# Optimization experiments

Hardware: AMD Instinct MI355X
Metric: run time of the kernel (lower is better)

## Reference

```python
import jax, jax.numpy as jnp
import numpy as np

HEADS = 8
HC = 64  # num_head_channels
DIM = 256
HIDDEN = HEADS * HC
EPS = 1e-5


def setup_inputs() -> dict:
    key = jax.random.key(0)
    ks = jax.random.split(key, 6)
    x = jax.random.normal(ks[0], (16, DIM, 64, 64), dtype=jnp.float32)
    Wq = jax.random.normal(ks[1], (HIDDEN, DIM), dtype=jnp.float32) * 0.02
    Wk = jax.random.normal(ks[2], (HIDDEN, DIM), dtype=jnp.float32) * 0.02
    Wv = jax.random.normal(ks[3], (HIDDEN, DIM), dtype=jnp.float32) * 0.02
    Wo = jax.random.normal(ks[4], (DIM, HIDDEN), dtype=jnp.float32) * 0.02
    bo = jnp.zeros((DIM,), dtype=jnp.float32)
    gamma = jnp.ones((DIM,), dtype=jnp.float32)
    beta = jnp.zeros((DIM,), dtype=jnp.float32)
    return {"x": x, "Wq": Wq, "Wk": Wk, "Wv": Wv, "Wo": Wo, "bo": bo,
            "gamma": gamma, "beta": beta}


def reference(x, Wq, Wk, Wv, Wo, bo, gamma, beta):
    b, c, h, w = x.shape
    n = h * w
    scale = HC ** (-0.5)
    xf = x.reshape(b, c, n)  # [b, c, n]
    # 1x1 convs == channel matmuls
    q = jnp.einsum('oc,bcn->bon', Wq, xf).reshape(b * HEADS, HC, n)
    k = jnp.einsum('oc,bcn->bon', Wk, xf).reshape(b * HEADS, HC, n)
    v = jnp.einsum('oc,bcn->bon', Wv, xf).reshape(b * HEADS, HC, n)
    q = jax.nn.softmax(q, axis=1) * scale      # softmax over head channels
    k = jax.nn.softmax(k, axis=2)              # softmax over spatial
    # context = k @ v^T : [bh, hc, hc]
    context = jnp.einsum('bdn,ben->bde', k, v)
    # output = context^T @ q : [bh, hc, n]
    out = jnp.einsum('bde,bdn->ben', context, q)
    out = out.reshape(b, HIDDEN, n)
    # to_out conv1x1 + bias
    y = jnp.einsum('oc,bcn->bon', Wo, out) + bo[None, :, None]
    # GroupNorm(num_groups=1): normalize over (c, n) per sample
    mean = jnp.mean(y, axis=(1, 2), keepdims=True)
    var = jnp.var(y, axis=(1, 2), keepdims=True)
    y = (y - mean) * jax.lax.rsqrt(var + EPS)
    y = y * gamma[None, :, None] + beta[None, :, None]
    return y.reshape(b, c, h, w) + x
```

## Files before the change

### kernel.cpp

```cpp
#include <hip/hip_runtime.h>
#include <hip/hip_bf16.h>

#define DEV __device__ __forceinline__

constexpr int B_ = 16, CDIM = 256, NDIM = 4096, HID = 512, HEADS = 8, HC = 64;
constexpr float EPSV = 1e-5f;

using bf16x8 = __attribute__((ext_vector_type(8))) __bf16;
using f32x4  = __attribute__((ext_vector_type(4))) float;
using s16x8  = __attribute__((ext_vector_type(8))) short;
using s16x4  = __attribute__((ext_vector_type(4))) short;

DEV short f2bf(float f) {
  __hip_bfloat16 h = __float2bfloat16(f);
  return *reinterpret_cast<short*>(&h);
}
DEV float bf2f(short s) {
  union { unsigned u; float f; } c;
  c.u = ((unsigned)(unsigned short)s) << 16;
  return c.f;
}
DEV f32x4 MFMA(bf16x8 a, bf16x8 b, f32x4 c) {
  return __builtin_amdgcn_mfma_f32_16x16x32_bf16(a, b, c, 0, 0, 0);
}

__global__ void wconv_kernel(const float* __restrict__ Wq, const float* __restrict__ Wk,
                             const float* __restrict__ Wv, const float* __restrict__ Wo,
                             short* __restrict__ Wall, short* __restrict__ Wo_b) {
  const int i = blockIdx.x * 256 + threadIdx.x;
  const int nw = HID * CDIM;
  if (i < nw) Wall[i] = f2bf(Wq[i]);
  else if (i < 2 * nw) Wall[i] = f2bf(Wk[i - nw]);
  else if (i < 3 * nw) Wall[i] = f2bf(Wv[i - 2 * nw]);
  if (i < CDIM * HID) Wo_b[i] = f2bf(Wo[i]);
}

__global__ __launch_bounds__(256) void xconv_kernel(const float* __restrict__ x, short* __restrict__ xt) {
  __shared__ float t[32][33];
  const int bi = blockIdx.z, n0 = blockIdx.x * 32, c0 = blockIdx.y * 32;
  const int tx = threadIdx.x, ty = threadIdx.y;
  const float* xb = x + (size_t)bi * CDIM * NDIM;
#pragma unroll
  for (int i = 0; i < 32; i += 8)
    t[ty + i][tx] = xb[(size_t)(c0 + ty + i) * NDIM + n0 + tx];
  __syncthreads();
  short* xtb = xt + (size_t)bi * NDIM * CDIM;
#pragma unroll
  for (int i = 0; i < 32; i += 8)
    xtb[(size_t)(n0 + ty + i) * CDIM + c0 + tx] = f2bf(t[tx][ty + i]);
}

DEV bf16x8 xs_read(const char* xs, int row, int colShorts) {
  int byte = (row << 9) + (colShorts << 1);
  byte ^= (row & 7) << 4;
  return *(const bf16x8*)(xs + byte);
}
DEV bf16x8 t128_read(const char* t, int row, int colShorts) {
  int byte = (row << 7) + (colShorts << 1);
  byte ^= (row & 7) << 4;
  return *(const bf16x8*)(t + byte);
}

__global__ __launch_bounds__(256) void kvslice_kernel(const short* __restrict__ Wall,
                                                      const short* __restrict__ xt,
                                                      float* __restrict__ ctxp,
                                                      float* __restrict__ statp,
                                                      int nper) {
  const int phys = blockIdx.x, sl = blockIdx.y, nsl = gridDim.y;
  const int h = phys >> 4, bi = phys & 15;
  const int bh = bi * 8 + h;
  const int tid = threadIdx.x, lane = tid & 63, wid = tid >> 6;
  const int ro = lane & 15, g = lane >> 4, ko = g * 8;
  const short* Wk = Wall + (size_t)(HID + h * HC) * CDIM;
  const short* Wv = Wall + (size_t)(2 * HID + h * HC) * CDIM;
  const char* xbase = (const char*)(xt + ((size_t)bi * NDIM + (size_t)sl * nper) * CDIM);
  __shared__ __align__(16) char xs[64 * 512];
  __shared__ short pl[64][68];
  __shared__ short vl[64][68];
  bf16x8 ak[8], av[8];
#pragma unroll
  for (int ks = 0; ks < 8; ++ks) {
    ak[ks] = *(const bf16x8*)&Wk[(size_t)(wid * 16 + ro) * CDIM + ks * 32 + ko];
    av[ks] = *(const bf16x8*)&Wv[(size_t)(wid * 16 + ro) * CDIM + ks * 32 + ko];
  }
  float ssum = 0.f;
  f32x4 cacc[4] = {};
  const int myrow = wid * 16 + ro;
  const int drow = wid * 16 + g * 4;
  s16x8 r[8];
#pragma unroll
  for (int it = 0; it < 8; ++it) r[it] = *(const s16x8*)(xbase + it * 4096 + tid * 16);
  for (int nc = 0; nc < nper; nc += 64) {
    if (nc > 0) {
#pragma unroll
      for (int ks = 0; ks < 2; ++ks) {
        bf16x8 pa = *(const bf16x8*)&pl[wid * 16 + ro][ks * 32 + ko];
#pragma unroll
        for (int et = 0; et < 4; ++et) {
          bf16x8 vb = *(const bf16x8*)&vl[et * 16 + ro][ks * 32 + ko];
          cacc[et] = MFMA(pa, vb, cacc[et]);
        }
      }
    }
#pragma unroll
    for (int it = 0; it < 8; ++it) {
      const int fb = it * 4096 + tid * 16;
      *(s16x8*)(xs + (fb ^ (((fb >> 9) & 7) << 4))) = r[it];
    }
    __syncthreads();
    if (nc + 64 < nper) {
      const char* srcn = xbase + (size_t)(nc + 64) * 512;
#pragma unroll
      for (int it = 0; it < 8; ++it) r[it] = *(const s16x8*)(srcn + it * 4096 + tid * 16);
    }
    f32x4 kacc[4] = {};
    f32x4 vacc[4] = {};
#pragma unroll
    for (int ks = 0; ks < 8; ++ks)
#pragma unroll
      for (int nt = 0; nt < 4; ++nt) {
        bf16x8 bfr = xs_read(xs, nt * 16 + ro, ks * 32 + ko);
        kacc[nt] = MFMA(bfr, ak[ks], kacc[nt]);
        vacc[nt] = MFMA(bfr, av[ks], vacc[nt]);
      }
#pragma unroll
    for (int nt = 0; nt < 4; ++nt) {
      s16x4 pv, vv;
#pragma unroll
      for (int j = 0; j < 4; ++j) {
        const float p = __expf(kacc[nt][j]);
        ssum += p;
        pv[j] = f2bf(p);
        vv[j] = f2bf(vacc[nt][j]);
      }
      *(s16x4*)&pl[myrow][nt * 16 + g * 4] = pv;
      *(s16x4*)&vl[myrow][nt * 16 + g * 4] = vv;
    }
    __syncthreads();
  }
#pragma unroll
  for (int ks = 0; ks < 2; ++ks) {
    bf16x8 pa = *(const bf16x8*)&pl[wid * 16 + ro][ks * 32 + ko];
#pragma unroll
    for (int et = 0; et < 4; ++et) {
      bf16x8 vb = *(const bf16x8*)&vl[et * 16 + ro][ks * 32 + ko];
      cacc[et] = MFMA(pa, vb, cacc[et]);
    }
  }
  ssum += __shfl_xor(ssum, 16);
  ssum += __shfl_xor(ssum, 32);
  float* cp = ctxp + ((size_t)bh * nsl + sl) * HC * HC;
#pragma unroll
  for (int et = 0; et < 4; ++et)
#pragma unroll
    for (int j = 0; j < 4; ++j)
      cp[(drow + j) * HC + et * 16 + ro] = cacc[et][j];
  if (g == 0) {
    float* sp = statp + ((size_t)bh * nsl + sl) * HC;
    sp[myrow] = ssum;
  }
}

__global__ __launch_bounds__(256) void qsm_kernel(const short* __restrict__ Wall,
                                                  const short* __restrict__ xt,
                                                  short* __restrict__ qtc,
                                                  int NC, int nbase) {
  const int bi = blockIdx.y, n0 = blockIdx.x * 64;
  const int tid = threadIdx.x, lane = tid & 63, wid = tid >> 6;
  const int ro = lane & 15, g = lane >> 4, ko = g * 8;
  __shared__ __align__(16) char xs[64 * 512];
  __shared__ short qtile[64][68];
  __shared__ float ps[4][4][16];
  const char* xbase = (const char*)(xt + ((size_t)bi * NDIM + nbase + n0) * CDIM);
#pragma unroll
  for (int it = 0; it < 8; ++it) {
    const int fb = it * 4096 + tid * 16;
    *(s16x8*)(xs + (fb ^ (((fb >> 9) & 7) << 4))) = *(const s16x8*)(xbase + fb);
  }
  __syncthreads();
  const short* wbase = Wall + (size_t)(wid * 16 + ro) * CDIM + ko;
  bf16x8 aq[8], aqn[8];
#pragma unroll
  for (int ks = 0; ks < 8; ++ks) aq[ks] = *(const bf16x8*)(wbase + ks * 32);
#pragma unroll 1
  for (int h = 0; h < HEADS; ++h) {
    if (h < 7) {
      const short* wn = wbase + (size_t)(h + 1) * HC * CDIM;
#pragma unroll
      for (int ks = 0; ks < 8; ++ks) aqn[ks] = *(const bf16x8*)(wn + ks * 32);
    }
    f32x4 kacc[4] = {};
#pragma unroll
    for (int ks = 0; ks < 8; ++ks)
#pragma unroll
      for (int nt = 0; nt < 4; ++nt)
        kacc[nt] = MFMA(aq[ks], xs_read(xs, nt * 16 + ro, ks * 32 + ko), kacc[nt]);
    float tsum[4];
#pragma unroll
    for (int nt = 0; nt < 4; ++nt) {
#pragma unroll
      for (int j = 0; j < 4; ++j) kacc[nt][j] = __expf(kacc[nt][j]);
      tsum[nt] = kacc[nt][0] + kacc[nt][1] + kacc[nt][2] + kacc[nt][3];
    }
#pragma unroll
    for (int nt = 0; nt < 4; ++nt) {
      tsum[nt] += __shfl_xor(tsum[nt], 16);
      tsum[nt] += __shfl_xor(tsum[nt], 32);
    }
    if (g == 0) {
#pragma unroll
      for (int nt = 0; nt < 4; ++nt) ps[wid][nt][ro] = tsum[nt];
    }
#pragma unroll
    for (int nt = 0; nt < 4; ++nt) {
      s16x4 v;
#pragma unroll
      for (int j = 0; j < 4; ++j) v[j] = f2bf(kacc[nt][j]);
      *(s16x4*)&qtile[nt * 16 + ro][wid * 16 + g * 4] = v;
    }
    __syncthreads();
    {
      const int row = tid >> 2, cb = (tid & 3) * 16;
      const int ntr = row >> 4, ror = row & 15;
      const float t = ps[0][ntr][ror] + ps[1][ntr][ror] + ps[2][ntr][ror] + ps[3][ntr][ror];
      const float inv = 0.125f / t;
      short* dst = qtc + ((size_t)bi * NC + n0 + row) * HID + h * HC + cb;
      s16x8 o0, o1;
#pragma unroll
      for (int jj = 0; jj < 8; ++jj) o0[jj] = f2bf(bf2f(qtile[row][cb + jj]) * inv);
#pragma unroll
      for (int jj = 0; jj < 8; ++jj) o1[jj] = f2bf(bf2f(qtile[row][cb + 8 + jj]) * inv);
      *(s16x8*)dst = o0;
      *(s16x8*)(dst + 8) = o1;
    }
    __syncthreads();
#pragma unroll
    for (int ks = 0; ks < 8; ++ks) aq[ks] = aqn[ks];
  }
}

__global__ __launch_bounds__(256) void cmred_kernel(const float* __restrict__ ctxp,
                                                    const float* __restrict__ statp,
                                                    const short* __restrict__ Wo_b,
                                                    short* __restrict__ Meff, int nsl) {
  const int bh = blockIdx.x, bi = bh >> 3, h = bh & 7;
  const int tid = threadIdx.x, lane = tid & 63, wid = tid >> 6;
  const int ro = lane & 15, ko = (lane >> 4) * 8;
  __shared__ short cl[64][68];
  {
    const int d = tid >> 2, eb = (tid & 3) * 16;
    const float* sp = statp + (size_t)bh * nsl * HC;
    float stot = 0.f;
    for (int i = 0; i < nsl; ++i) stot += sp[i * HC + d];
    const float inv = 1.f / stot;
    const float* cp = ctxp + (size_t)bh * nsl * HC * HC + d * HC + eb;
#pragma unroll
    for (int e4 = 0; e4 < 16; e4 += 4) {
      float u0 = 0.f, u1 = 0.f, u2 = 0.f, u3 = 0.f;
      for (int i = 0; i < nsl; ++i) {
        const float4 c = *(const float4*)&cp[i * HC * HC + e4];
        u0 += c.x; u1 += c.y; u2 += c.z; u3 += c.w;
      }
      cl[d][eb + e4 + 0] = f2bf(u0 * inv);
      cl[d][eb + e4 + 1] = f2bf(u1 * inv);
      cl[d][eb + e4 + 2] = f2bf(u2 * inv);
      cl[d][eb + e4 + 3] = f2bf(u3 * inv);
    }
  }
  __syncthreads();
  const short* Arow = Wo_b + h * HC;
  f32x4 acc[4][4] = {};
#pragma unroll
  for (int ks = 0; ks < 64; ks += 32) {
    bf16x8 af[4], bv[4];
#pragma unroll
    for (int mi = 0; mi < 4; ++mi)
      af[mi] = *(const bf16x8*)&Arow[(size_t)(wid * 64 + mi * 16 + ro) * HID + ks + ko];
#pragma unroll
    for (int ni = 0; ni < 4; ++ni)
      bv[ni] = *(const bf16x8*)&cl[ni * 16 + ro][ks + ko];
#pragma unroll
    for (int mi = 0; mi < 4; ++mi)
#pragma unroll
      for (int ni = 0; ni < 4; ++ni) acc[mi][ni] = MFMA(af[mi], bv[ni], acc[mi][ni]);
  }
  short* Mb = Meff + (size_t)bi * CDIM * HID + h * HC;
  const int r0 = wid * 64 + ((lane >> 4) << 2), c0 = lane & 15;
#pragma unroll
  for (int mi = 0; mi < 4; ++mi)
#pragma unroll
    for (int ni = 0; ni < 4; ++ni)
#pragma unroll
      for (int j = 0; j < 4; ++j)
        Mb[(size_t)(r0 + mi * 16 + j) * HID + ni * 16 + c0] = f2bf(acc[mi][ni][j]);
}

template <bool BF16OUT>
__global__ __launch_bounds__(256) void ymm_kernel(const short* __restrict__ Meff,
                                                  const short* __restrict__ qtc,
                                                  const float* __restrict__ bo,
                                                  void* __restrict__ yout,
                                                  float2* __restrict__ partials,
                                                  int NC, int nbase, int pbase, int swz) {
  constexpr int K = HID;
  __shared__ __align__(16) char Al[128 * 128];
  __shared__ __align__(16) char Bl[128 * 128];
  __shared__ float a1[4], a2[4];
  int bi, mt, nt;
  if (swz) {
    const int lin = blockIdx.x + 32 * blockIdx.y + 64 * blockIdx.z;
    bi = ((lin & 7) << 1) | (lin >> 9);
    const int rest = (lin >> 3) & 63;
    mt = rest >> 5;
    nt = rest & 31;
  } else {
    bi = blockIdx.z; mt = blockIdx.y; nt = blockIdx.x;
  }
  const int tid = threadIdx.x, lane = tid & 63, wid = tid >> 6;
  const int wr = (wid >> 1) * 64, wc = (wid & 1) * 64;
  const char* Ab = (const char*)(Meff + (size_t)bi * CDIM * HID + (size_t)mt * 128 * K);
  const char* Bb = (const char*)(qtc + ((size_t)bi * NC + (size_t)nt * 128) * K);
  f32x4 acc[4][4] = {};
  const int ro = lane & 15, ko = (lane >> 4) * 8;
  for (int kt = 0; kt < K; kt += 64) {
    const char* As = Ab + kt * 2;
    const char* Bs = Bb + kt * 2;
#pragma unroll
    for (int it = 0; it < 4; ++it) {
      const int fb = it * 4096 + tid * 16;
      const int row = fb >> 7, inner = fb & 127;
      const int swb = fb ^ ((row & 7) << 4);
      *(s16x8*)(Al + swb) = *(const s16x8*)(As + (size_t)row * 1024 + inner);
      *(s16x8*)(Bl + swb) = *(const s16x8*)(Bs + (size_t)row * 1024 + inner);
    }
    __syncthreads();
#pragma unroll
    for (int ks = 0; ks < 64; ks += 32) {
      bf16x8 af[4], bfr[4];
#pragma unroll
      for (int i = 0; i < 4; ++i) {
        af[i]  = t128_read(Al, wr + i * 16 + ro, ks + ko);
        bfr[i] = t128_read(Bl, wc + i * 16 + ro, ks + ko);
      }
#pragma unroll
      for (int mi = 0; mi < 4; ++mi)
#pragma unroll
        for (int ni = 0; ni < 4; ++ni)
          acc[mi][ni] = MFMA(af[mi], bfr[ni], acc[mi][ni]);
    }
    __syncthreads();
  }
  const int r0 = mt * 128 + wr + ((lane >> 4) << 2);
  const int c0 = nbase + nt * 128 + wc + ro;
  float s1 = 0.f, s2 = 0.f;
#pragma unroll
  for (int mi = 0; mi < 4; ++mi)
#pragma unroll
    for (int j = 0; j < 4; ++j) {
      const int row = r0 + mi * 16 + j;
      const float b = bo[row];
#pragma unroll
      for (int ni = 0; ni < 4; ++ni) {
        const float v = acc[mi][ni][j] + b;
        if constexpr (BF16OUT)
          ((short*)yout)[(size_t)bi * CDIM * NDIM + (size_t)row * NDIM + c0 + ni * 16] = f2bf(v);
        else
          ((float*)yout)[(size_t)bi * CDIM * NDIM + (size_t)row * NDIM + c0 + ni * 16] = v;
        s1 += v;
        s2 += v * v;
      }
    }
#pragma unroll
  for (int o = 1; o < 64; o <<= 1) { s1 += __shfl_xor(s1, o); s2 += __shfl_xor(s2, o); }
  if (lane == 0) { a1[wid] = s1; a2[wid] = s2; }
  __syncthreads();
  if (tid == 0)
    partials[bi * 64 + pbase + mt * gridDim.x + nt] =
        make_float2(a1[0] + a1[1] + a1[2] + a1[3], a2[0] + a2[1] + a2[2] + a2[3]);
}

__global__ void redstats_kernel(const float2* __restrict__ partials, float* __restrict__ stats) {
  const int bi = blockIdx.x, l = threadIdx.x;
  float2 p = partials[bi * 64 + l];
  float s1 = p.x, s2 = p.y;
#pragma unroll
  for (int o = 32; o; o >>= 1) { s1 += __shfl_xor(s1, o); s2 += __shfl_xor(s2, o); }
  if (l == 0) { stats[bi * 2] = s1; stats[bi * 2 + 1] = s2; }
}

template <bool YBF>
__global__ __launch_bounds__(256) void final_kernel(const void* __restrict__ ysrc, float* __restrict__ dst,
                                                    const float* __restrict__ x,
                                                    const float* __restrict__ gamma, const float* __restrict__ beta,
                                                    const float* __restrict__ stats) {
  const int bi = blockIdx.y;
  constexpr float invN = 1.f / ((float)CDIM * NDIM);
  const float mean = stats[bi * 2] * invN;
  const float var = stats[bi * 2 + 1] * invN - mean * mean;
  const float rstd = rsqrtf(var + EPSV);
  float4* d4 = (float4*)(dst + (size_t)bi * CDIM * NDIM);
  const float4* x4 = (const float4*)(x + (size_t)bi * CDIM * NDIM);
  for (int i = blockIdx.x * 256 + threadIdx.x; i < CDIM * NDIM / 4; i += 128 * 256) {
    const int c = i >> 10;
    const float g = gamma[c] * rstd;
    const float b = beta[c] - mean * g;
    float4 v;
    if constexpr (YBF) {
      s16x4 yv = *(const s16x4*)((const short*)ysrc + (size_t)bi * CDIM * NDIM + (size_t)i * 4);
      v.x = bf2f(yv[0]); v.y = bf2f(yv[1]); v.z = bf2f(yv[2]); v.w = bf2f(yv[3]);
    } else {
      v = ((const float4*)((const float*)ysrc + (size_t)bi * CDIM * NDIM))[i];
    }
    const float4 xv = x4[i];
    v.x = v.x * g + b + xv.x;
    v.y = v.y * g + b + xv.y;
    v.z = v.z * g + b + xv.z;
    v.w = v.w * g + b + xv.w;
    d4[i] = v;
  }
}

extern "C" void kernel_launch(void* const* d_in, const int* in_sizes, int n_in,
                              void* d_out, int out_size, void* d_ws, size_t ws_size,
                              hipStream_t stream) {
  const float* x     = (const float*)d_in[0];
  const float* Wq    = (const float*)d_in[1];
  const float* Wk    = (const float*)d_in[2];
  const float* Wv    = (const float*)d_in[3];
  const float* Wo    = (const float*)d_in[4];
  const float* bo    = (const float*)d_in[5];
  const float* gamma = (const float*)d_in[6];
  const float* beta  = (const float*)d_in[7];
  float* out = (float*)d_out;

  char* w = (char*)d_ws;
  size_t off = 0;
  auto alloc = [&](size_t n) {
    char* p = w + off;
    off = (off + n + 255) & ~(size_t)255;
    return p;
  };
  constexpr int NSL = 8;
  short* xt    = (short*)alloc((size_t)B_ * NDIM * CDIM * 2);
  short* Wall  = (short*)alloc((size_t)3 * HID * CDIM * 2);
  short* Wo_b  = (short*)alloc((size_t)CDIM * HID * 2);
  short* Meff  = (short*)alloc((size_t)B_ * CDIM * HID * 2);
  float2* partials = (float2*)alloc((size_t)B_ * 64 * sizeof(float2));
  float* stats = (float*)alloc(32 * 4);
  float* ctxp  = (float*)alloc((size_t)128 * NSL * HC * HC * 4);
  float* statp = (float*)alloc((size_t)128 * NSL * HC * 4);
  const size_t base = off;

  int NC = 4096;
  while (NC > 64 && base + (size_t)B_ * NC * HID * 2 > ws_size) NC >>= 1;
  short* qtc = (short*)alloc((size_t)B_ * NC * HID * 2);
  const size_t ybf_bytes = (size_t)B_ * CDIM * NDIM * 2;
  const bool use_ybf = (off + ybf_bytes) <= ws_size;
  short* ybf = use_ybf ? (short*)alloc(ybf_bytes) : nullptr;

  wconv_kernel<<<1536, 256, 0, stream>>>(Wq, Wk, Wv, Wo, Wall, Wo_b);
  xconv_kernel<<<dim3(128, 8, B_), dim3(32, 8), 0, stream>>>(x, xt);
  kvslice_kernel<<<dim3(128, NSL), 256, 0, stream>>>(Wall, xt, ctxp, statp, NDIM / NSL);
  cmred_kernel<<<128, 256, 0, stream>>>(ctxp, statp, Wo_b, Meff, NSL);
  const int nchunks = NDIM / NC;
  for (int c = 0; c < nchunks; ++c) {
    const int swz = (NC == 4096) ? 1 : 0;
    qsm_kernel<<<dim3(NC / 64, B_), 256, 0, stream>>>(Wall, xt, qtc, NC, c * NC);
    if (use_ybf)
      ymm_kernel<true><<<dim3(NC / 128, 2, B_), 256, 0, stream>>>(Meff, qtc, bo, ybf, partials,
                                                                  NC, c * NC, c * 2 * (NC / 128), swz);
    else
      ymm_kernel<false><<<dim3(NC / 128, 2, B_), 256, 0, stream>>>(Meff, qtc, bo, out, partials,
                                                                   NC, c * NC, c * 2 * (NC / 128), swz);
  }
  redstats_kernel<<<B_, 64, 0, stream>>>(partials, stats);
  if (use_ybf)
    final_kernel<true><<<dim3(128, B_), 256, 0, stream>>>(ybf, out, x, gamma, beta, stats);
  else
    final_kernel<false><<<dim3(128, B_), 256, 0, stream>>>(out, out, x, gamma, beta, stats);
}
```

Measured before the change: 190.3 us.

## Fuse q-softmax projection into output matmul and add MFMA priority hints

Replaces the separate q-softmax kernel and the Meff×q output matmul with one fused kernel. Each block computes q for a 64-column tile over two head groups, keeps the normalized q in LDS, and multiplies by Meff directly, so the large qtc intermediate is never written to or read from global memory. It also adds s_setprio around MFMA regions in kvslice and moves the barrier after the next-tile prefetch issue. In exchange, each block reloads Wq and Meff fragments from global/L2 per tile, uses smaller output tiles, and holds 32 accumulator vectors per thread, which raises register pressure.

```diff
diff --git a/kernel.cpp b/kernel.cpp
--- a/kernel.cpp
+++ b/kernel.cpp
@@ -55,10 +55,10 @@
   byte ^= (row & 7) << 4;
   return *(const bf16x8*)(xs + byte);
 }
-DEV bf16x8 t128_read(const char* t, int row, int colShorts) {
-  int byte = (row << 7) + (colShorts << 1);
+DEV void tile512_write4(char* t, int row, int colShorts, s16x4 v) {
+  int byte = (row << 9) + (colShorts << 1);
   byte ^= (row & 7) << 4;
-  return *(const bf16x8*)(t + byte);
+  *(s16x4*)(t + byte) = v;
 }
 
 __global__ __launch_bounds__(256) void kvslice_kernel(const short* __restrict__ Wall,
@@ -92,6 +92,7 @@
   for (int it = 0; it < 8; ++it) r[it] = *(const s16x8*)(xbase + it * 4096 + tid * 16);
   for (int nc = 0; nc < nper; nc += 64) {
     if (nc > 0) {
+      __builtin_amdgcn_s_setprio(1);
 #pragma unroll
       for (int ks = 0; ks < 2; ++ks) {
         bf16x8 pa = *(const bf16x8*)&pl[wid * 16 + ro][ks * 32 + ko];
@@ -101,20 +102,22 @@
           cacc[et] = MFMA(pa, vb, cacc[et]);
         }
       }
+      __builtin_amdgcn_s_setprio(0);
     }
 #pragma unroll
     for (int it = 0; it < 8; ++it) {
       const int fb = it * 4096 + tid * 16;
       *(s16x8*)(xs + (fb ^ (((fb >> 9) & 7) << 4))) = r[it];
     }
-    __syncthreads();
     if (nc + 64 < nper) {
       const char* srcn = xbase + (size_t)(nc + 64) * 512;
 #pragma unroll
       for (int it = 0; it < 8; ++it) r[it] = *(const s16x8*)(srcn + it * 4096 + tid * 16);
     }
+    __syncthreads();
     f32x4 kacc[4] = {};
     f32x4 vacc[4] = {};
+    __builtin_amdgcn_s_setprio(1);
 #pragma unroll
     for (int ks = 0; ks < 8; ++ks)
 #pragma unroll
@@ -123,6 +126,7 @@
         kacc[nt] = MFMA(bfr, ak[ks], kacc[nt]);
         vacc[nt] = MFMA(bfr, av[ks], vacc[nt]);
       }
+    __builtin_amdgcn_s_setprio(0);
 #pragma unroll
     for (int nt = 0; nt < 4; ++nt) {
       s16x4 pv, vv;
@@ -158,84 +162,6 @@
   if (g == 0) {
     float* sp = statp + ((size_t)bh * nsl + sl) * HC;
     sp[myrow] = ssum;
-  }
-}
-
-__global__ __launch_bounds__(256) void qsm_kernel(const short* __restrict__ Wall,
-                                                  const short* __restrict__ xt,
-                                                  short* __restrict__ qtc,
-                                                  int NC, int nbase) {
-  const int bi = blockIdx.y, n0 = blockIdx.x * 64;
-  const int tid = threadIdx.x, lane = tid & 63, wid = tid >> 6;
-  const int ro = lane & 15, g = lane >> 4, ko = g * 8;
-  __shared__ __align__(16) char xs[64 * 512];
-  __shared__ short qtile[64][68];
-  __shared__ float ps[4][4][16];
-  const char* xbase = (const char*)(xt + ((size_t)bi * NDIM + nbase + n0) * CDIM);
-#pragma unroll
-  for (int it = 0; it < 8; ++it) {
-    const int fb = it * 4096 + tid * 16;
-    *(s16x8*)(xs + (fb ^ (((fb >> 9) & 7) << 4))) = *(const s16x8*)(xbase + fb);
-  }
-  __syncthreads();
-  const short* wbase = Wall + (size_t)(wid * 16 + ro) * CDIM + ko;
-  bf16x8 aq[8], aqn[8];
-#pragma unroll
-  for (int ks = 0; ks < 8; ++ks) aq[ks] = *(const bf16x8*)(wbase + ks * 32);
-#pragma unroll 1
-  for (int h = 0; h < HEADS; ++h) {
-    if (h < 7) {
-      const short* wn = wbase + (size_t)(h + 1) * HC * CDIM;
-#pragma unroll
-      for (int ks = 0; ks < 8; ++ks) aqn[ks] = *(const bf16x8*)(wn + ks * 32);
-    }
-    f32x4 kacc[4] = {};
-#pragma unroll
-    for (int ks = 0; ks < 8; ++ks)
-#pragma unroll
-      for (int nt = 0; nt < 4; ++nt)
-        kacc[nt] = MFMA(aq[ks], xs_read(xs, nt * 16 + ro, ks * 32 + ko), kacc[nt]);
-    float tsum[4];
-#pragma unroll
-    for (int nt = 0; nt < 4; ++nt) {
-#pragma unroll
-      for (int j = 0; j < 4; ++j) kacc[nt][j] = __expf(kacc[nt][j]);
-      tsum[nt] = kacc[nt][0] + kacc[nt][1] + kacc[nt][2] + kacc[nt][3];
-    }
-#pragma unroll
-    for (int nt = 0; nt < 4; ++nt) {
-      tsum[nt] += __shfl_xor(tsum[nt], 16);
-      tsum[nt] += __shfl_xor(tsum[nt], 32);
-    }
-    if (g == 0) {
-#pragma unroll
-      for (int nt = 0; nt < 4; ++nt) ps[wid][nt][ro] = tsum[nt];
-    }
-#pragma unroll
-    for (int nt = 0; nt < 4; ++nt) {
-      s16x4 v;
-#pragma unroll
-      for (int j = 0; j < 4; ++j) v[j] = f2bf(kacc[nt][j]);
-      *(s16x4*)&qtile[nt * 16 + ro][wid * 16 + g * 4] = v;
-    }
-    __syncthreads();
-    {
-      const int row = tid >> 2, cb = (tid & 3) * 16;
-      const int ntr = row >> 4, ror = row & 15;
-      const float t = ps[0][ntr][ror] + ps[1][ntr][ror] + ps[2][ntr][ror] + ps[3][ntr][ror];
-      const float inv = 0.125f / t;
-      short* dst = qtc + ((size_t)bi * NC + n0 + row) * HID + h * HC + cb;
-      s16x8 o0, o1;
-#pragma unroll
-      for (int jj = 0; jj < 8; ++jj) o0[jj] = f2bf(bf2f(qtile[row][cb + jj]) * inv);
-#pragma unroll
-      for (int jj = 0; jj < 8; ++jj) o1[jj] = f2bf(bf2f(qtile[row][cb + 8 + jj]) * inv);
-      *(s16x8*)dst = o0;
-      *(s16x8*)(dst + 8) = o1;
-    }
-    __syncthreads();
-#pragma unroll
-    for (int ks = 0; ks < 8; ++ks) aq[ks] = aqn[ks];
   }
 }
 
@@ -296,86 +222,121 @@
 }
 
 template <bool BF16OUT>
-__global__ __launch_bounds__(256) void ymm_kernel(const short* __restrict__ Meff,
-                                                  const short* __restrict__ qtc,
-                                                  const float* __restrict__ bo,
-                                                  void* __restrict__ yout,
-                                                  float2* __restrict__ partials,
-                                                  int NC, int nbase, int pbase, int swz) {
-  constexpr int K = HID;
-  __shared__ __align__(16) char Al[128 * 128];
-  __shared__ __align__(16) char Bl[128 * 128];
+__global__ __launch_bounds__(256) void qymm_kernel(const short* __restrict__ Wall,
+                                                   const short* __restrict__ xt,
+                                                   const short* __restrict__ Meff,
+                                                   const float* __restrict__ bo,
+                                                   void* __restrict__ yout,
+                                                   float2* __restrict__ partials) {
+  const int bx = blockIdx.x;
+  const int bi = bx & 15, nt = bx >> 4;
+  const int n0 = nt * 64;
+  const int tid = threadIdx.x, lane = tid & 63, wid = tid >> 6;
+  const int ro = lane & 15, g = lane >> 4, ko = g * 8;
+  __shared__ __align__(16) char xs[64 * 512];
+  __shared__ __align__(16) char ql[64 * 512];
   __shared__ float a1[4], a2[4];
-  int bi, mt, nt;
-  if (swz) {
-    const int lin = blockIdx.x + 32 * blockIdx.y + 64 * blockIdx.z;
-    bi = ((lin & 7) << 1) | (lin >> 9);
-    const int rest = (lin >> 3) & 63;
-    mt = rest >> 5;
-    nt = rest & 31;
-  } else {
-    bi = blockIdx.z; mt = blockIdx.y; nt = blockIdx.x;
-  }
-  const int tid = threadIdx.x, lane = tid & 63, wid = tid >> 6;
-  const int wr = (wid >> 1) * 64, wc = (wid & 1) * 64;
-  const char* Ab = (const char*)(Meff + (size_t)bi * CDIM * HID + (size_t)mt * 128 * K);
-  const char* Bb = (const char*)(qtc + ((size_t)bi * NC + (size_t)nt * 128) * K);
-  f32x4 acc[4][4] = {};
-  const int ro = lane & 15, ko = (lane >> 4) * 8;
-  for (int kt = 0; kt < K; kt += 64) {
-    const char* As = Ab + kt * 2;
-    const char* Bs = Bb + kt * 2;
-#pragma unroll
-    for (int it = 0; it < 4; ++it) {
-      const int fb = it * 4096 + tid * 16;
-      const int row = fb >> 7, inner = fb & 127;
-      const int swb = fb ^ ((row & 7) << 4);
-      *(s16x8*)(Al + swb) = *(const s16x8*)(As + (size_t)row * 1024 + inner);
-      *(s16x8*)(Bl + swb) = *(const s16x8*)(Bs + (size_t)row * 1024 + inner);
+  const char* xbase = (const char*)(xt + ((size_t)bi * NDIM + n0) * CDIM);
+#pragma unroll
+  for (int it = 0; it < 8; ++it) {
+    const int fb = it * 4096 + tid * 16;
+    *(s16x8*)(xs + (fb ^ (((fb >> 9) & 7) << 4))) = *(const s16x8*)(xbase + fb);
+  }
+  __syncthreads();
+
+  const short* Mb = Meff + (size_t)bi * CDIM * HID;
+  f32x4 acc2[4][4] = {};
+
+#pragma unroll 1
+  for (int p = 0; p < 2; ++p) {
+    const int head = p * 4 + wid;
+    const short* Wq = Wall + (size_t)head * HC * CDIM;
+    f32x4 qa[4][4] = {};
+    __builtin_amdgcn_s_setprio(1);
+#pragma unroll
+    for (int ks = 0; ks < 8; ++ks) {
+      bf16x8 af[4];
+#pragma unroll
+      for (int rt = 0; rt < 4; ++rt)
+        af[rt] = *(const bf16x8*)&Wq[(size_t)(rt * 16 + ro) * CDIM + ks * 32 + ko];
+#pragma unroll
+      for (int nti = 0; nti < 4; ++nti) {
+        bf16x8 bfr = xs_read(xs, nti * 16 + ro, ks * 32 + ko);
+#pragma unroll
+        for (int rt = 0; rt < 4; ++rt) qa[rt][nti] = MFMA(af[rt], bfr, qa[rt][nti]);
+      }
+    }
+    __builtin_amdgcn_s_setprio(0);
+    float sm[4];
+#pragma unroll
+    for (int nti = 0; nti < 4; ++nti) {
+      float t = 0.f;
+#pragma unroll
+      for (int rt = 0; rt < 4; ++rt)
+#pragma unroll
+        for (int j = 0; j < 4; ++j) {
+          qa[rt][nti][j] = __expf(qa[rt][nti][j]);
+          t += qa[rt][nti][j];
+        }
+      t += __shfl_xor(t, 16);
+      t += __shfl_xor(t, 32);
+      sm[nti] = 0.125f / t;
+    }
+#pragma unroll
+    for (int nti = 0; nti < 4; ++nti) {
+      const int nrow = nti * 16 + ro;
+#pragma unroll
+      for (int rt = 0; rt < 4; ++rt) {
+        s16x4 v;
+#pragma unroll
+        for (int j = 0; j < 4; ++j) v[j] = f2bf(qa[rt][nti][j] * sm[nti]);
+        tile512_write4(ql, nrow, wid * 64 + rt * 16 + g * 4, v);
+      }
     }
     __syncthreads();
-#pragma unroll
-    for (int ks = 0; ks < 64; ks += 32) {
-      bf16x8 af[4], bfr[4];
-#pragma unroll
-      for (int i = 0; i < 4; ++i) {
-        af[i]  = t128_read(Al, wr + i * 16 + ro, ks + ko);
-        bfr[i] = t128_read(Bl, wc + i * 16 + ro, ks + ko);
-      }
-#pragma unroll
-      for (int mi = 0; mi < 4; ++mi)
-#pragma unroll
-        for (int ni = 0; ni < 4; ++ni)
-          acc[mi][ni] = MFMA(af[mi], bfr[ni], acc[mi][ni]);
-    }
+    __builtin_amdgcn_s_setprio(1);
+#pragma unroll
+    for (int ks = 0; ks < 8; ++ks) {
+      bf16x8 am[4], bq[4];
+#pragma unroll
+      for (int rt = 0; rt < 4; ++rt)
+        am[rt] = *(const bf16x8*)&Mb[(size_t)(wid * 64 + rt * 16 + ro) * HID +
+                                     p * 256 + ks * 32 + ko];
+#pragma unroll
+      for (int nti = 0; nti < 4; ++nti) bq[nti] = xs_read(ql, nti * 16 + ro, ks * 32 + ko);
+#pragma unroll
+      for (int rt = 0; rt < 4; ++rt)
+#pragma unroll
+        for (int nti = 0; nti < 4; ++nti) acc2[rt][nti] = MFMA(am[rt], bq[nti], acc2[rt][nti]);
+    }
+    __builtin_amdgcn_s_setprio(0);
     __syncthreads();
   }
-  const int r0 = mt * 128 + wr + ((lane >> 4) << 2);
-  const int c0 = nbase + nt * 128 + wc + ro;
   float s1 = 0.f, s2 = 0.f;
 #pragma unroll
-  for (int mi = 0; mi < 4; ++mi)
+  for (int rt = 0; rt < 4; ++rt) {
 #pragma unroll
     for (int j = 0; j < 4; ++j) {
-      const int row = r0 + mi * 16 + j;
-      const float b = bo[row];
-#pragma unroll
-      for (int ni = 0; ni < 4; ++ni) {
-        const float v = acc[mi][ni][j] + b;
+      const int orow = wid * 64 + rt * 16 + g * 4 + j;
+      const float b = bo[orow];
+#pragma unroll
+      for (int nti = 0; nti < 4; ++nti) {
+        const float v = acc2[rt][nti][j] + b;
         if constexpr (BF16OUT)
-          ((short*)yout)[(size_t)bi * CDIM * NDIM + (size_t)row * NDIM + c0 + ni * 16] = f2bf(v);
+          ((short*)yout)[(size_t)bi * CDIM * NDIM + (size_t)orow * NDIM + n0 + nti * 16 + ro] = f2bf(v);
         else
-          ((float*)yout)[(size_t)bi * CDIM * NDIM + (size_t)row * NDIM + c0 + ni * 16] = v;
+          ((float*)yout)[(size_t)bi * CDIM * NDIM + (size_t)orow * NDIM + n0 + nti * 16 + ro] = v;
         s1 += v;
         s2 += v * v;
       }
     }
+  }
 #pragma unroll
   for (int o = 1; o < 64; o <<= 1) { s1 += __shfl_xor(s1, o); s2 += __shfl_xor(s2, o); }
   if (lane == 0) { a1[wid] = s1; a2[wid] = s2; }
   __syncthreads();
   if (tid == 0)
-    partials[bi * 64 + pbase + mt * gridDim.x + nt] =
+    partials[bi * 64 + nt] =
         make_float2(a1[0] + a1[1] + a1[2] + a1[3], a2[0] + a2[1] + a2[2] + a2[3]);
 }
 
@@ -449,11 +410,7 @@
   float* stats = (float*)alloc(32 * 4);
   float* ctxp  = (float*)alloc((size_t)128 * NSL * HC * HC * 4);
   float* statp = (float*)alloc((size_t)128 * NSL * HC * 4);
-  const size_t base = off;
-
-  int NC = 4096;
-  while (NC > 64 && base + (size_t)B_ * NC * HID * 2 > ws_size) NC >>= 1;
-  short* qtc = (short*)alloc((size_t)B_ * NC * HID * 2);
+
   const size_t ybf_bytes = (size_t)B_ * CDIM * NDIM * 2;
   const bool use_ybf = (off + ybf_bytes) <= ws_size;
   short* ybf = use_ybf ? (short*)alloc(ybf_bytes) : nullptr;
@@ -462,17 +419,10 @@
   xconv_kernel<<<dim3(128, 8, B_), dim3(32, 8), 0, stream>>>(x, xt);
   kvslice_kernel<<<dim3(128, NSL), 256, 0, stream>>>(Wall, xt, ctxp, statp, NDIM / NSL);
   cmred_kernel<<<128, 256, 0, stream>>>(ctxp, statp, Wo_b, Meff, NSL);
-  const int nchunks = NDIM / NC;
-  for (int c = 0; c < nchunks; ++c) {
-    const int swz = (NC == 4096) ? 1 : 0;
-    qsm_kernel<<<dim3(NC / 64, B_), 256, 0, stream>>>(Wall, xt, qtc, NC, c * NC);
-    if (use_ybf)
-      ymm_kernel<true><<<dim3(NC / 128, 2, B_), 256, 0, stream>>>(Meff, qtc, bo, ybf, partials,
-                                                                  NC, c * NC, c * 2 * (NC / 128), swz);
-    else
-      ymm_kernel<false><<<dim3(NC / 128, 2, B_), 256, 0, stream>>>(Meff, qtc, bo, out, partials,
-                                                                   NC, c * NC, c * 2 * (NC / 128), swz);
-  }
+  if (use_ybf)
+    qymm_kernel<true><<<1024, 256, 0, stream>>>(Wall, xt, Meff, bo, ybf, partials);
+  else
+    qymm_kernel<false><<<1024, 256, 0, stream>>>(Wall, xt, Meff, bo, out, partials);
   redstats_kernel<<<B_, 64, 0, stream>>>(partials, stats);
   if (use_ybf)
     final_kernel<true><<<dim3(128, B_), 256, 0, stream>>>(ybf, out, x, gamma, beta, stats);
```

Measured after the change: 193.8 us. Within noise of the previous version (+1.9%).
